# Performance work log

Hardware: AMD Instinct MI355X
Metric: run time of the kernel (lower is better)

The kernel has to match this reference:

```python
import jax, jax.numpy as jnp
import numpy as np

N_ATOMS = 50000
N_EDGES = 800000
EMB = 128      # emb_size_atom
EMB_BF = 128   # emb_size_bf
N_HIDDEN = 3
INV_SQRT2 = 0.7071067811865476
SILU_SCALE = 1.0 / 0.6  # GemNet ScaledSiLU


def scaled_silu(x):
    return jax.nn.silu(x) * SILU_SCALE


def residual_layer(x, w0, w1):
    # ResidualLayer(units, nLayers=2): two bias-free Dense+ScaledSiLU, then inv_sqrt(2)*(x + y)
    y = scaled_silu(x @ w0)
    y = scaled_silu(y @ w1)
    return (x + y) * INV_SQRT2


def setup_inputs() -> dict:
    key = jax.random.key(0)
    ks = jax.random.split(key, 9)
    s_emb = 1.0 / np.float32(np.sqrt(EMB))
    s_bf = 1.0 / np.float32(np.sqrt(EMB_BF))
    return {
        "h": jax.random.normal(ks[0], (N_ATOMS, EMB), jnp.float32),
        "bf": jax.random.uniform(ks[1], (N_EDGES, EMB_BF), jnp.float32),
        "idx_s": jax.random.randint(ks[2], (N_EDGES,), 0, N_ATOMS, jnp.int64),
        "idx_t": jax.random.randint(ks[3], (N_EDGES,), 0, N_ATOMS, jnp.int64),
        "w_bf": jax.random.normal(ks[4], (EMB_BF, EMB), jnp.float32) * s_bf,
        "w_pre": jax.random.normal(ks[5], (2, EMB, EMB), jnp.float32) * s_emb,
        "w_mlp1": jax.random.normal(ks[6], (EMB, EMB), jnp.float32) * s_emb,
        "w_res": jax.random.normal(ks[7], (N_HIDDEN, 2, EMB, EMB), jnp.float32) * s_emb,
        "scale_sum": jnp.ones((1,), jnp.float32),  # ScalingFactor (1.0 without scale_file)
    }


def reference(h, bf, idx_s, idx_t, w_bf, w_pre, w_mlp1, w_res, scale_sum):
    # pre_residual
    h_res = residual_layer(h, w_pre[0], w_pre[1])          # (nAtoms, EMB)
    # dense_bf: bias-free linear, no activation
    mlp_bf = bf @ w_bf                                     # (nEdges, EMB)
    # gather source embeddings, Hadamard multiply with edge features
    x = h_res[idx_s] * mlp_bf                              # (nEdges, EMB)
    # scatter-sum over target atoms
    x2 = jax.ops.segment_sum(x, idx_t, num_segments=N_ATOMS)  # (nAtoms, EMB)
    x = x2 * scale_sum[0]
    # MLP: Dense+activation, then nHidden residual blocks
    x = scaled_silu(x @ w_mlp1)
    for i in range(N_HIDDEN):
        x = residual_layer(x, w_res[i, 0], w_res[i, 1])
    return x
```

## Files before the change

### kernel.cpp

```cpp
#include <hip/hip_runtime.h>

#define EMB 128
#define NATOMS 50000
#define NEDGES 800000
#define PADN 50176

typedef __attribute__((ext_vector_type(8))) short bf16x8;
typedef __attribute__((ext_vector_type(4))) float f32x4;

static const size_t H_RES_OFF  = 0;
static const size_t X2_OFF     = (size_t)NATOMS * EMB * 4;
static const size_t W_OFF      = 2 * (size_t)NATOMS * EMB * 4;
static const size_t FLAG_OFF   = W_OFF + 10 * 128 * 128 * 2;
static const size_t COUNTS_OFF = (FLAG_OFF + 4 + 255) & ~(size_t)255;
static const size_t SEG_OFF    = COUNTS_OFF + (size_t)PADN * 4;
static const size_t CURSOR_OFF = SEG_OFF + (size_t)PADN * 4;
static const size_t BSUM_OFF   = CURSOR_OFF + (size_t)PADN * 4;
static const size_t ORDER_OFF  = BSUM_OFF + 1024;

__device__ __forceinline__ short f2bf(float f) {
  unsigned u = __float_as_uint(f);
  u += 0x7fffu + ((u >> 16) & 1u);
  return (short)(u >> 16);
}

__device__ __forceinline__ float ssilu(float x) {
  return x * (1.0f / 0.6f) / (1.0f + __expf(-x));
}

__device__ __forceinline__ int xidx(int row, int k) {
  return (row << 7) + ((((k >> 2) ^ (row & 7)) << 2) | (k & 3));
}
__device__ __forceinline__ int bidx(int row, int k) {
  return (row << 7) + ((((k >> 3) ^ (row & 7)) << 3) | (k & 7));
}

__device__ __forceinline__ void stage_w(const short* __restrict__ src, short* dst) {
  const int wave = threadIdx.x >> 6;
  const int lane = threadIdx.x & 63;
  const char* s = (const char*)src;
  char* d = (char*)dst;
#pragma unroll
  for (int i = 0; i < 8; ++i) {
    const int off = wave * 8192 + i * 1024;
    __builtin_amdgcn_global_load_lds(
        (const __attribute__((address_space(1))) void*)(s + off + lane * 16),
        (__attribute__((address_space(3))) void*)(d + off), 16, 0, 0);
  }
}

__device__ __forceinline__ void stage_x(const float* __restrict__ src, int row0, float* x) {
#pragma unroll
  for (int i = 0; i < 8; ++i) {
    const int c = threadIdx.x + i * 256;
    const int row = c >> 5, unit = c & 31;
    f32x4 v = {0.f, 0.f, 0.f, 0.f};
    if (row0 + row < NATOMS) v = *(const f32x4*)(src + (size_t)(row0 + row) * EMB + unit * 4);
    *(f32x4*)&x[(row << 7) + ((unit ^ (row & 7)) << 2)] = v;
  }
}

template <bool SRC_BF16>
__device__ __forceinline__ void gemm_stage(const float* xsrc, const short* ysrc,
                                           const short* w, int wr0, int lr, int lh,
                                           f32x4* acc) {
#pragma unroll
  for (int kk = 0; kk < 4; ++kk) {
    const int k0 = kk * 32 + lh * 8;
    const int ra = wr0 + lr;
    bf16x8 a;
    if constexpr (SRC_BF16) {
      a = *(const bf16x8*)&ysrc[bidx(ra, k0)];
    } else {
      f32x4 u0 = *(const f32x4*)&xsrc[xidx(ra, k0)];
      f32x4 u1 = *(const f32x4*)&xsrc[xidx(ra, k0 + 4)];
      a[0] = f2bf(u0[0]); a[1] = f2bf(u0[1]); a[2] = f2bf(u0[2]); a[3] = f2bf(u0[3]);
      a[4] = f2bf(u1[0]); a[5] = f2bf(u1[1]); a[6] = f2bf(u1[2]); a[7] = f2bf(u1[3]);
    }
#pragma unroll
    for (int j0 = 0; j0 < 8; ++j0) {
      bf16x8 b = *(const bf16x8*)&w[bidx(j0 * 16 + lr, k0)];
      acc[j0] = __builtin_amdgcn_mfma_f32_16x16x32_bf16(a, b, acc[j0], 0, 0, 0);
    }
  }
}

__global__ void prep_weights(const float* __restrict__ wbf, const float* __restrict__ wpre,
                             const float* __restrict__ wmlp1, const float* __restrict__ wres,
                             short* __restrict__ W) {
  const int s = blockIdx.x >> 7;
  const int k = blockIdx.x & 127;
  const int n = threadIdx.x;
  const float* src;
  if (s == 0) src = wbf;
  else if (s <= 2) src = wpre + (s - 1) * 16384;
  else if (s == 3) src = wmlp1;
  else src = wres + (s - 4) * 16384;
  const float v = src[k * EMB + n];
  W[s * 16384 + (n << 7) + ((((k >> 3) ^ (n & 7)) << 3) | (k & 7))] = f2bf(v);
}

__global__ void detect_idx(const int* __restrict__ idx, int* __restrict__ flag) {
  if (threadIdx.x == 0 && blockIdx.x == 0) {
    int ornz = 0;
#pragma unroll
    for (int i = 0; i < 64; ++i) ornz |= idx[2 * i + 1];
    *flag = (ornz == 0) ? 1 : 0;
  }
}

__device__ __forceinline__ int load_idx(const void* p, int e, int f64) {
  return f64 ? (int)((const long long*)p)[e] : ((const int*)p)[e];
}

__global__ void hist_kernel(const void* __restrict__ idx_t_p, int* __restrict__ counts,
                            const int* __restrict__ flag) {
  const int e = blockIdx.x * 256 + threadIdx.x;
  if (e < NEDGES) atomicAdd(&counts[load_idx(idx_t_p, e, *flag)], 1);
}

__global__ void scan_blocks(const int* __restrict__ counts, int* __restrict__ seg,
                            int* __restrict__ bsum) {
  const int i = blockIdx.x * 256 + threadIdx.x;
  const int lane = threadIdx.x & 63, wave = threadIdx.x >> 6;
  const int v = counts[i];
  int incl = v;
#pragma unroll
  for (int d = 1; d < 64; d <<= 1) {
    int t = __shfl_up(incl, d, 64);
    if (lane >= d) incl += t;
  }
  __shared__ int wtot[4];
  if (lane == 63) wtot[wave] = incl;
  __syncthreads();
  int woff = 0;
  for (int w = 0; w < wave; ++w) woff += wtot[w];
  seg[i] = woff + incl - v;
  if (threadIdx.x == 255) bsum[blockIdx.x] = woff + incl;
}

__global__ void scan_top(int* __restrict__ bsum) {
  const int i = threadIdx.x;
  const int lane = i & 63, wave = i >> 6;
  const int v = (i < 196) ? bsum[i] : 0;
  int incl = v;
#pragma unroll
  for (int d = 1; d < 64; d <<= 1) {
    int t = __shfl_up(incl, d, 64);
    if (lane >= d) incl += t;
  }
  __shared__ int wtot[4];
  if (lane == 63) wtot[wave] = incl;
  __syncthreads();
  int woff = 0;
  for (int w = 0; w < wave; ++w) woff += wtot[w];
  if (i < 196) bsum[i] = woff + incl - v;
}

__global__ void add_off(int* __restrict__ seg, const int* __restrict__ bsum,
                        int* __restrict__ cursor) {
  const int i = blockIdx.x * 256 + threadIdx.x;
  const int s = seg[i] + bsum[blockIdx.x];
  seg[i] = s;
  cursor[i] = s;
}

__global__ void scatter_kernel(const void* __restrict__ idx_t_p, int* __restrict__ cursor,
                               int* __restrict__ order, const int* __restrict__ flag) {
  const int e = blockIdx.x * 256 + threadIdx.x;
  if (e < NEDGES) {
    const int t = load_idx(idx_t_p, e, *flag);
    const int pos = atomicAdd(&cursor[t], 1);
    order[pos] = e;
  }
}

__global__ __launch_bounds__(256, 2) void atom_pre(const float* __restrict__ h,
                                                   float* __restrict__ h_res,
                                                   const short* __restrict__ W) {
  __shared__ float x_lds[64 * 128];
  __shared__ short y_lds[64 * 128];
  __shared__ short w_lds[128 * 128];
  const int lane = threadIdx.x & 63, wave = threadIdx.x >> 6;
  const int lr = lane & 15, lh = lane >> 4;
  const int row0 = blockIdx.x * 64, wr0 = wave * 16;
  const f32x4 vzero = {0.f, 0.f, 0.f, 0.f};

  stage_x(h, row0, x_lds);
  stage_w(W + 1 * 16384, w_lds);
  __syncthreads();

  f32x4 acc[8];
#pragma unroll
  for (int j = 0; j < 8; ++j) acc[j] = vzero;
  gemm_stage<false>(x_lds, nullptr, w_lds, wr0, lr, lh, acc);
#pragma unroll
  for (int j0 = 0; j0 < 8; ++j0)
#pragma unroll
    for (int j = 0; j < 4; ++j)
      y_lds[bidx(wr0 + lh * 4 + j, j0 * 16 + lr)] = f2bf(ssilu(acc[j0][j]));

  __syncthreads();
  stage_w(W + 2 * 16384, w_lds);
  __syncthreads();

#pragma unroll
  for (int j = 0; j < 8; ++j) acc[j] = vzero;
  gemm_stage<true>(nullptr, y_lds, w_lds, wr0, lr, lh, acc);

#pragma unroll
  for (int j = 0; j < 4; ++j) {
    const int row = wr0 + lh * 4 + j;
    const int ga = row0 + row;
    if (ga < NATOMS) {
#pragma unroll
      for (int j0 = 0; j0 < 8; ++j0) {
        const int col = j0 * 16 + lr;
        h_res[(size_t)ga * EMB + col] =
            (x_lds[xidx(row, col)] + ssilu(acc[j0][j])) * 0.70710678118654752440f;
      }
    }
  }
}

__global__ __launch_bounds__(256) void edge_atom(const float* __restrict__ bf,
                                                 const float* __restrict__ h_res,
                                                 const void* __restrict__ idx_s_p,
                                                 const int* __restrict__ seg,
                                                 const int* __restrict__ order,
                                                 const short* __restrict__ W,
                                                 float* __restrict__ x2,
                                                 const int* __restrict__ flag) {
  __shared__ short w_lds[128 * 128];
  const int lane = threadIdx.x & 63, wave = threadIdx.x >> 6;
  const int lr = lane & 15, lh = lane >> 4;
  const int f64 = *flag;

  stage_w(W, w_lds);
  __syncthreads();

  const int gwid = blockIdx.x * 4 + wave;
  const int nw = gridDim.x * 4;
  const f32x4 vzero = {0.f, 0.f, 0.f, 0.f};

  for (int t = gwid; t < NATOMS; t += nw) {
    const int s0 = seg[t], s1 = seg[t + 1];
    float psum[8] = {0.f, 0.f, 0.f, 0.f, 0.f, 0.f, 0.f, 0.f};

    for (int c0 = s0; c0 < s1; c0 += 16) {
      const int rem = s1 - c0;
      int e = 0, is = 0;
      const bool rowok = (lr < rem);
      if (rowok) {
        e = order[c0 + lr];
        is = load_idx(idx_s_p, e, f64);
      }
      f32x4 acc[8];
#pragma unroll
      for (int j = 0; j < 8; ++j) acc[j] = vzero;

#pragma unroll
      for (int kk = 0; kk < 4; ++kk) {
        bf16x8 a = {0, 0, 0, 0, 0, 0, 0, 0};
        if (rowok) {
          const float* p = bf + (size_t)e * EMB + kk * 32 + lh * 8;
          f32x4 u0 = *(const f32x4*)p;
          f32x4 u1 = *(const f32x4*)(p + 4);
          a[0] = f2bf(u0[0]); a[1] = f2bf(u0[1]); a[2] = f2bf(u0[2]); a[3] = f2bf(u0[3]);
          a[4] = f2bf(u1[0]); a[5] = f2bf(u1[1]); a[6] = f2bf(u1[2]); a[7] = f2bf(u1[3]);
        }
#pragma unroll
        for (int j0 = 0; j0 < 8; ++j0) {
          bf16x8 b = *(const bf16x8*)&w_lds[bidx(j0 * 16 + lr, kk * 32 + lh * 8)];
          acc[j0] = __builtin_amdgcn_mfma_f32_16x16x32_bf16(a, b, acc[j0], 0, 0, 0);
        }
      }

#pragma unroll
      for (int j = 0; j < 4; ++j) {
        const int row = 4 * lh + j;
        const int src = (lh << 4) | row;
        const int isj = __shfl(is, src, 64);
        if (row < rem) {
          const float* hrow = h_res + (size_t)isj * EMB;
#pragma unroll
          for (int j0 = 0; j0 < 8; ++j0)
            psum[j0] += acc[j0][j] * hrow[j0 * 16 + lr];
        }
      }
    }

#pragma unroll
    for (int j0 = 0; j0 < 8; ++j0) {
      float r = psum[j0];
      r += __shfl_xor(r, 16, 64);
      r += __shfl_xor(r, 32, 64);
      psum[j0] = r;
    }
    if (lane < 16) {
#pragma unroll
      for (int j0 = 0; j0 < 8; ++j0)
        x2[(size_t)t * EMB + j0 * 16 + lane] = psum[j0];
    }
  }
}

__global__ __launch_bounds__(256, 2) void atom_post(const float* __restrict__ x2,
                                                    float* __restrict__ out,
                                                    const short* __restrict__ W,
                                                    const float* __restrict__ scale_sum) {
  __shared__ float x_lds[64 * 128];
  __shared__ short y_lds[64 * 128];
  __shared__ short w_lds[128 * 128];
  const int lane = threadIdx.x & 63, wave = threadIdx.x >> 6;
  const int lr = lane & 15, lh = lane >> 4;
  const int row0 = blockIdx.x * 64, wr0 = wave * 16;
  const float sc = scale_sum[0];
  const f32x4 vzero = {0.f, 0.f, 0.f, 0.f};

  stage_x(x2, row0, x_lds);
  stage_w(W + 3 * 16384, w_lds);
  __syncthreads();

  f32x4 acc[8];
#pragma unroll
  for (int j = 0; j < 8; ++j) acc[j] = vzero;
  gemm_stage<false>(x_lds, nullptr, w_lds, wr0, lr, lh, acc);
#pragma unroll
  for (int j0 = 0; j0 < 8; ++j0)
#pragma unroll
    for (int j = 0; j < 4; ++j)
      x_lds[xidx(wr0 + lh * 4 + j, j0 * 16 + lr)] = ssilu(acc[j0][j] * sc);

  for (int L = 0; L < 3; ++L) {
    __syncthreads();
    stage_w(W + (size_t)(4 + 2 * L) * 16384, w_lds);
    __syncthreads();
#pragma unroll
    for (int j = 0; j < 8; ++j) acc[j] = vzero;
    gemm_stage<false>(x_lds, nullptr, w_lds, wr0, lr, lh, acc);
#pragma unroll
    for (int j0 = 0; j0 < 8; ++j0)
#pragma unroll
      for (int j = 0; j < 4; ++j)
        y_lds[bidx(wr0 + lh * 4 + j, j0 * 16 + lr)] = f2bf(ssilu(acc[j0][j]));

    __syncthreads();
    stage_w(W + (size_t)(5 + 2 * L) * 16384, w_lds);
    __syncthreads();
#pragma unroll
    for (int j = 0; j < 8; ++j) acc[j] = vzero;
    gemm_stage<true>(nullptr, y_lds, w_lds, wr0, lr, lh, acc);

    if (L < 2) {
#pragma unroll
      for (int j = 0; j < 4; ++j) {
        const int row = wr0 + lh * 4 + j;
#pragma unroll
        for (int j0 = 0; j0 < 8; ++j0) {
          const int col = j0 * 16 + lr;
          const float xv = x_lds[xidx(row, col)];
          x_lds[xidx(row, col)] = (xv + ssilu(acc[j0][j])) * 0.70710678118654752440f;
        }
      }
    } else {
#pragma unroll
      for (int j = 0; j < 4; ++j) {
        const int row = wr0 + lh * 4 + j;
        const int ga = row0 + row;
        if (ga < NATOMS) {
#pragma unroll
          for (int j0 = 0; j0 < 8; ++j0) {
            const int col = j0 * 16 + lr;
            out[(size_t)ga * EMB + col] =
                (x_lds[xidx(row, col)] + ssilu(acc[j0][j])) * 0.70710678118654752440f;
          }
        }
      }
    }
  }
}

extern "C" void kernel_launch(void* const* d_in, const int* in_sizes, int n_in,
                              void* d_out, int out_size, void* d_ws, size_t ws_size,
                              hipStream_t stream) {
  const float* h      = (const float*)d_in[0];
  const float* bf     = (const float*)d_in[1];
  const void*  idx_s  = d_in[2];
  const void*  idx_t  = d_in[3];
  const float* w_bf   = (const float*)d_in[4];
  const float* w_pre  = (const float*)d_in[5];
  const float* w_mlp1 = (const float*)d_in[6];
  const float* w_res  = (const float*)d_in[7];
  const float* scale  = (const float*)d_in[8];
  float* out = (float*)d_out;

  char* ws = (char*)d_ws;
  float* h_res  = (float*)(ws + H_RES_OFF);
  float* x2     = (float*)(ws + X2_OFF);
  short* W      = (short*)(ws + W_OFF);
  int*   flag   = (int*)(ws + FLAG_OFF);
  int*   counts = (int*)(ws + COUNTS_OFF);
  int*   segp   = (int*)(ws + SEG_OFF);
  int*   cursor = (int*)(ws + CURSOR_OFF);
  int*   bsum   = (int*)(ws + BSUM_OFF);
  int*   order  = (int*)(ws + ORDER_OFF);

  hipMemsetAsync(counts, 0, (size_t)PADN * 4, stream);
  prep_weights<<<dim3(10 * 128), dim3(128), 0, stream>>>(w_bf, w_pre, w_mlp1, w_res, W);
  detect_idx<<<dim3(1), dim3(64), 0, stream>>>((const int*)idx_s, flag);

  hist_kernel<<<dim3(NEDGES / 256), dim3(256), 0, stream>>>(idx_t, counts, flag);
  scan_blocks<<<dim3(PADN / 256), dim3(256), 0, stream>>>(counts, segp, bsum);
  scan_top<<<dim3(1), dim3(256), 0, stream>>>(bsum);
  add_off<<<dim3(PADN / 256), dim3(256), 0, stream>>>(segp, bsum, cursor);
  scatter_kernel<<<dim3(NEDGES / 256), dim3(256), 0, stream>>>(idx_t, cursor, order, flag);

  atom_pre<<<dim3((NATOMS + 63) / 64), dim3(256), 0, stream>>>(h, h_res, W);
  edge_atom<<<dim3(2048), dim3(256), 0, stream>>>(bf, h_res, idx_s, segp, order, W, x2, flag);
  atom_post<<<dim3((NATOMS + 63) / 64), dim3(256), 0, stream>>>(x2, out, W, scale);
}
```

Before: 437.2 us.

## Split edge work into fixed 32-edge chunks with segmented reduction and atomics

Replaces the per-atom wave loop, where waves walk variable-length segments in 16-edge steps with partially masked MFMAs, with a fixed edge-parallel decomposition. Each wave takes 32 sorted edges and runs full MFMA tiles. It then reduces runs of equal target atoms with ballot, writing directly when the segment lies entirely inside the chunk and using atomicAdd otherwise. This removes load imbalance and wasted MFMA lanes on short segments, at the cost of zeroing x2 beforehand, extra atomics at chunk boundaries, and a serial per-run loop. detect_idx also switches to a wave-wide ballot.

Result: faster. 356.3 us (median of 5 runs) (-18.5%).

```diff
diff --git a/kernel.cpp b/kernel.cpp
--- a/kernel.cpp
+++ b/kernel.cpp
@@ -101,12 +101,10 @@
 }
 
 __global__ void detect_idx(const int* __restrict__ idx, int* __restrict__ flag) {
-  if (threadIdx.x == 0 && blockIdx.x == 0) {
-    int ornz = 0;
-#pragma unroll
-    for (int i = 0; i < 64; ++i) ornz |= idx[2 * i + 1];
-    *flag = (ornz == 0) ? 1 : 0;
-  }
+  const int lane = threadIdx.x & 63;
+  const int v = idx[2 * lane + 1];
+  const unsigned long long nz = __ballot(v != 0);
+  if (lane == 0) *flag = (nz == 0ull) ? 1 : 0;
 }
 
 __device__ __forceinline__ int load_idx(const void* p, int e, int f64) {
@@ -223,14 +221,15 @@
   }
 }
 
-__global__ __launch_bounds__(256) void edge_atom(const float* __restrict__ bf,
-                                                 const float* __restrict__ h_res,
-                                                 const void* __restrict__ idx_s_p,
-                                                 const int* __restrict__ seg,
-                                                 const int* __restrict__ order,
-                                                 const short* __restrict__ W,
-                                                 float* __restrict__ x2,
-                                                 const int* __restrict__ flag) {
+__global__ __launch_bounds__(256, 4) void edge_sorted(const float* __restrict__ bf,
+                                                      const float* __restrict__ h_res,
+                                                      const void* __restrict__ idx_s_p,
+                                                      const void* __restrict__ idx_t_p,
+                                                      const int* __restrict__ seg,
+                                                      const int* __restrict__ order,
+                                                      const short* __restrict__ W,
+                                                      float* __restrict__ x2,
+                                                      const int* __restrict__ flag) {
   __shared__ short w_lds[128 * 128];
   const int lane = threadIdx.x & 63, wave = threadIdx.x >> 6;
   const int lr = lane & 15, lh = lane >> 4;
@@ -239,69 +238,99 @@
   stage_w(W, w_lds);
   __syncthreads();
 
-  const int gwid = blockIdx.x * 4 + wave;
-  const int nw = gridDim.x * 4;
+  const int p0 = blockIdx.x * 128 + wave * 32;
+  const int r32 = lane & 31;
+  const int e_mine = order[p0 + r32];
+  const int is_mine = load_idx(idx_s_p, e_mine, f64);
+  const int it_mine = load_idx(idx_t_p, e_mine, f64);
+
+  const int e_rf0 = __shfl(e_mine, lr, 64);
+  const int e_rf1 = __shfl(e_mine, 16 + lr, 64);
+
+  bf16x8 a_all[2][4];
+#pragma unroll
+  for (int kk = 0; kk < 4; ++kk) {
+#pragma unroll
+    for (int rf = 0; rf < 2; ++rf) {
+      const int e = rf ? e_rf1 : e_rf0;
+      const float* p = bf + (size_t)e * EMB + kk * 32 + lh * 8;
+      f32x4 u0 = *(const f32x4*)p;
+      f32x4 u1 = *(const f32x4*)(p + 4);
+      bf16x8 a;
+      a[0] = f2bf(u0[0]); a[1] = f2bf(u0[1]); a[2] = f2bf(u0[2]); a[3] = f2bf(u0[3]);
+      a[4] = f2bf(u1[0]); a[5] = f2bf(u1[1]); a[6] = f2bf(u1[2]); a[7] = f2bf(u1[3]);
+      a_all[rf][kk] = a;
+    }
+  }
+
+  f32x4 acc[2][8];
   const f32x4 vzero = {0.f, 0.f, 0.f, 0.f};
-
-  for (int t = gwid; t < NATOMS; t += nw) {
-    const int s0 = seg[t], s1 = seg[t + 1];
+#pragma unroll
+  for (int rf = 0; rf < 2; ++rf)
+#pragma unroll
+    for (int j0 = 0; j0 < 8; ++j0) acc[rf][j0] = vzero;
+
+#pragma unroll
+  for (int kk = 0; kk < 4; ++kk) {
+#pragma unroll
+    for (int j0 = 0; j0 < 8; ++j0) {
+      bf16x8 b = *(const bf16x8*)&w_lds[bidx(j0 * 16 + lr, kk * 32 + lh * 8)];
+      acc[0][j0] = __builtin_amdgcn_mfma_f32_16x16x32_bf16(a_all[0][kk], b, acc[0][j0], 0, 0, 0);
+      acc[1][j0] = __builtin_amdgcn_mfma_f32_16x16x32_bf16(a_all[1][kk], b, acc[1][j0], 0, 0, 0);
+    }
+  }
+
+#pragma unroll
+  for (int rf = 0; rf < 2; ++rf) {
+#pragma unroll
+    for (int j = 0; j < 4; ++j) {
+      const int isj = __shfl(is_mine, rf * 16 + 4 * lh + j, 64);
+      const float* hrow = h_res + (size_t)isj * EMB;
+#pragma unroll
+      for (int j0 = 0; j0 < 8; ++j0)
+        acc[rf][j0][j] *= hrow[j0 * 16 + lr];
+    }
+  }
+
+  int r = 0;
+  while (r < 32) {
+    const int t = __shfl(it_mine, r, 64);
+    const unsigned long long bal = __ballot(it_mine == t);
+    const unsigned long long m = (bal & 0xffffffffull) >> r;
+    const int cnt = (int)__builtin_ctzll(~m);
+    const int end = r + cnt;
+
     float psum[8] = {0.f, 0.f, 0.f, 0.f, 0.f, 0.f, 0.f, 0.f};
-
-    for (int c0 = s0; c0 < s1; c0 += 16) {
-      const int rem = s1 - c0;
-      int e = 0, is = 0;
-      const bool rowok = (lr < rem);
-      if (rowok) {
-        e = order[c0 + lr];
-        is = load_idx(idx_s_p, e, f64);
-      }
-      f32x4 acc[8];
-#pragma unroll
-      for (int j = 0; j < 8; ++j) acc[j] = vzero;
-
-#pragma unroll
-      for (int kk = 0; kk < 4; ++kk) {
-        bf16x8 a = {0, 0, 0, 0, 0, 0, 0, 0};
-        if (rowok) {
-          const float* p = bf + (size_t)e * EMB + kk * 32 + lh * 8;
-          f32x4 u0 = *(const f32x4*)p;
-          f32x4 u1 = *(const f32x4*)(p + 4);
-          a[0] = f2bf(u0[0]); a[1] = f2bf(u0[1]); a[2] = f2bf(u0[2]); a[3] = f2bf(u0[3]);
-          a[4] = f2bf(u1[0]); a[5] = f2bf(u1[1]); a[6] = f2bf(u1[2]); a[7] = f2bf(u1[3]);
-        }
-#pragma unroll
-        for (int j0 = 0; j0 < 8; ++j0) {
-          bf16x8 b = *(const bf16x8*)&w_lds[bidx(j0 * 16 + lr, kk * 32 + lh * 8)];
-          acc[j0] = __builtin_amdgcn_mfma_f32_16x16x32_bf16(a, b, acc[j0], 0, 0, 0);
+#pragma unroll
+    for (int rf = 0; rf < 2; ++rf) {
+#pragma unroll
+      for (int j = 0; j < 4; ++j) {
+        const int row = rf * 16 + 4 * lh + j;
+        if (row >= r && row < end) {
+#pragma unroll
+          for (int j0 = 0; j0 < 8; ++j0) psum[j0] += acc[rf][j0][j];
         }
       }
-
-#pragma unroll
-      for (int j = 0; j < 4; ++j) {
-        const int row = 4 * lh + j;
-        const int src = (lh << 4) | row;
-        const int isj = __shfl(is, src, 64);
-        if (row < rem) {
-          const float* hrow = h_res + (size_t)isj * EMB;
-#pragma unroll
-          for (int j0 = 0; j0 < 8; ++j0)
-            psum[j0] += acc[j0][j] * hrow[j0 * 16 + lr];
-        }
+    }
+#pragma unroll
+    for (int j0 = 0; j0 < 8; ++j0) {
+      psum[j0] += __shfl_xor(psum[j0], 16, 64);
+      psum[j0] += __shfl_xor(psum[j0], 32, 64);
+    }
+
+    const int s0 = seg[t], s1 = seg[t + 1];
+    const bool interior = (s0 == p0 + r) && (s1 == p0 + end);
+    if (lane < 16) {
+      float* orow = x2 + (size_t)t * EMB;
+      if (interior) {
+#pragma unroll
+        for (int j0 = 0; j0 < 8; ++j0) orow[j0 * 16 + lane] = psum[j0];
+      } else {
+#pragma unroll
+        for (int j0 = 0; j0 < 8; ++j0) atomicAdd(&orow[j0 * 16 + lane], psum[j0]);
       }
     }
-
-#pragma unroll
-    for (int j0 = 0; j0 < 8; ++j0) {
-      float r = psum[j0];
-      r += __shfl_xor(r, 16, 64);
-      r += __shfl_xor(r, 32, 64);
-      psum[j0] = r;
-    }
-    if (lane < 16) {
-#pragma unroll
-      for (int j0 = 0; j0 < 8; ++j0)
-        x2[(size_t)t * EMB + j0 * 16 + lane] = psum[j0];
-    }
+    r = end;
   }
 }
 
@@ -407,6 +436,7 @@
   int*   order  = (int*)(ws + ORDER_OFF);
 
   hipMemsetAsync(counts, 0, (size_t)PADN * 4, stream);
+  hipMemsetAsync(x2, 0, (size_t)NATOMS * EMB * 4, stream);
   prep_weights<<<dim3(10 * 128), dim3(128), 0, stream>>>(w_bf, w_pre, w_mlp1, w_res, W);
   detect_idx<<<dim3(1), dim3(64), 0, stream>>>((const int*)idx_s, flag);
 
@@ -417,6 +447,7 @@
   scatter_kernel<<<dim3(NEDGES / 256), dim3(256), 0, stream>>>(idx_t, cursor, order, flag);
 
   atom_pre<<<dim3((NATOMS + 63) / 64), dim3(256), 0, stream>>>(h, h_res, W);
-  edge_atom<<<dim3(2048), dim3(256), 0, stream>>>(bf, h_res, idx_s, segp, order, W, x2, flag);
+  edge_sorted<<<dim3(NEDGES / 128), dim3(256), 0, stream>>>(bf, h_res, idx_s, idx_t, segp,
+                                                            order, W, x2, flag);
   atom_post<<<dim3((NATOMS + 63) / 64), dim3(256), 0, stream>>>(x2, out, W, scale);
 }
```
